# Kernel tuning notes

Hardware: AMD Instinct MI355X
Metric: run time of the kernel (lower is better)

## Reference

```python
import jax, jax.numpy as jnp
import numpy as np

N, F_IN, F_OUT, N_HEAD = 4096, 256, 64, 4
EDGE_P = 0.01  # sparsity of the random adjacency


def setup_inputs() -> dict:
    key = jax.random.key(0)
    k_h, k_adj, k_w, k_as, k_ad = jax.random.split(key, 5)
    h = jax.random.normal(k_h, (N, F_IN), dtype=jnp.float32)
    # random boolean adjacency with self-loops so every softmax row is valid
    adj = jax.random.uniform(k_adj, (N, N)) < EDGE_P
    adj = adj | jnp.eye(N, dtype=bool)
    # xavier_uniform-style params
    lim_w = float(np.sqrt(6.0 / (F_IN + F_OUT)))
    lim_a = float(np.sqrt(6.0 / (F_OUT + 1)))
    w = jax.random.uniform(k_w, (N_HEAD, F_IN, F_OUT), minval=-lim_w, maxval=lim_w, dtype=jnp.float32)
    a_src = jax.random.uniform(k_as, (N_HEAD, F_OUT, 1), minval=-lim_a, maxval=lim_a, dtype=jnp.float32)
    a_dst = jax.random.uniform(k_ad, (N_HEAD, F_OUT, 1), minval=-lim_a, maxval=lim_a, dtype=jnp.float32)
    bias = jnp.zeros((F_OUT,), dtype=jnp.float32)
    return {"h": h, "adj": adj, "w": w, "a_src": a_src, "a_dst": a_dst, "bias": bias}


def reference(h, adj, w, a_src, a_dst, bias):
    # h_prime[k] = h @ w[k]  -> [H, n, f_out]
    h_prime = jnp.einsum('nf,hfo->hno', h, w)
    # attention logits: attn[k,i,j] = src[k,i] + dst[k,j]
    src = jnp.einsum('hno,ho->hn', h_prime, a_src[..., 0])  # [H, n]
    dst = jnp.einsum('hno,ho->hn', h_prime, a_dst[..., 0])  # [H, n]
    scores = src[:, :, None] + dst[:, None, :]              # [H, n, n]
    scores = jnp.where(scores >= 0, scores, 0.2 * scores)   # leaky_relu(0.2)
    neg = jnp.asarray(jnp.finfo(scores.dtype).min, scores.dtype)
    scores = jnp.where(adj[None, :, :], scores, neg)
    attn = jax.nn.softmax(scores, axis=-1)                  # [H, n, n]
    out = jnp.einsum('hij,hjo->iho', attn, h_prime)         # [n, H, f_out]
    return out + bias
```

## Files before the change

### kernel.cpp

```cpp
#include <hip/hip_runtime.h>

#define NN 4096
#define FIN 256
#define FOUT 64
#define NH 4
#define CAP 128
#define MFB 256
#define CPB 1024

typedef __attribute__((ext_vector_type(8))) short bf16x8;
typedef __attribute__((ext_vector_type(4))) float f32x4;

__device__ __forceinline__ unsigned short f2bf(float f) {
    unsigned u = __float_as_uint(f);
    u = (u + 0x7fff + ((u >> 16) & 1)) >> 16;
    return (unsigned short)u;
}
__device__ __forceinline__ float bf2f(unsigned short s) {
    return __uint_as_float((unsigned)s << 16);
}

__global__ __launch_bounds__(256) void gat_prep(
    const float* __restrict__ h, const int* __restrict__ adj,
    const float* __restrict__ w, const float* __restrict__ a_src,
    const float* __restrict__ a_dst,
    unsigned short* __restrict__ hb, float* __restrict__ sd,
    unsigned long long* __restrict__ bits)
{
    const int b = blockIdx.x, t = threadIdx.x;
    const int wv = t >> 6, lane = t & 63;

    __shared__ bf16x8 bfrag[2048];

    if (b < MFB) {
        const int head = b & 3, n0 = (b >> 2) * 64;
        const int lrow = lane & 15, lk8 = lane >> 4;

        const float* hrow = h + (size_t)(n0 + wv * 16 + lrow) * FIN + lk8 * 8;
        bf16x8 a[8];
#pragma unroll
        for (int ks = 0; ks < 8; ++ks) {
            const float4 v0 = *(const float4*)(hrow + ks * 32);
            const float4 v1 = *(const float4*)(hrow + ks * 32 + 4);
            union { bf16x8 v; unsigned short s[8]; } u;
            u.s[0] = f2bf(v0.x); u.s[1] = f2bf(v0.y);
            u.s[2] = f2bf(v0.z); u.s[3] = f2bf(v0.w);
            u.s[4] = f2bf(v1.x); u.s[5] = f2bf(v1.y);
            u.s[6] = f2bf(v1.z); u.s[7] = f2bf(v1.w);
            a[ks] = u.v;
        }

#pragma unroll
        for (int i = 0; i < 8; ++i) {
            const int g = t + i * 256;
            const int lg = g & 63, ks = (g >> 6) & 7, nt = g >> 9;
            const int col = nt * 16 + (lg & 15);
            const int kbase = ks * 32 + (lg >> 4) * 8;
            const float* wp = w + ((size_t)head * FIN + kbase) * FOUT + col;
            union { bf16x8 v; unsigned short s[8]; } u;
#pragma unroll
            for (int j = 0; j < 8; ++j) u.s[j] = f2bf(wp[j * FOUT]);
            bfrag[g] = u.v;
        }
        __syncthreads();

        f32x4 acc[4] = {{0.f,0.f,0.f,0.f},{0.f,0.f,0.f,0.f},
                        {0.f,0.f,0.f,0.f},{0.f,0.f,0.f,0.f}};
#pragma unroll
        for (int ks = 0; ks < 8; ++ks) {
#pragma unroll
            for (int nt = 0; nt < 4; ++nt)
                acc[nt] = __builtin_amdgcn_mfma_f32_16x16x32_bf16(
                              a[ks], bfrag[(nt * 8 + ks) * 64 + lane], acc[nt], 0, 0, 0);
        }

        const int mbase = n0 + wv * 16 + lk8 * 4;
#pragma unroll
        for (int nt = 0; nt < 4; ++nt)
#pragma unroll
            for (int r = 0; r < 4; ++r)
                hb[((size_t)head * NN + mbase + r) * FOUT + nt * 16 + lrow] =
                    f2bf(acc[nt][r]);

        float as_nt[4], ad_nt[4];
#pragma unroll
        for (int nt = 0; nt < 4; ++nt) {
            as_nt[nt] = a_src[head * FOUT + nt * 16 + lrow];
            ad_nt[nt] = a_dst[head * FOUT + nt * 16 + lrow];
        }
        float psr[4] = {0.f,0.f,0.f,0.f}, pdr[4] = {0.f,0.f,0.f,0.f};
#pragma unroll
        for (int nt = 0; nt < 4; ++nt)
#pragma unroll
            for (int r = 0; r < 4; ++r) {
                psr[r] = fmaf(acc[nt][r], as_nt[nt], psr[r]);
                pdr[r] = fmaf(acc[nt][r], ad_nt[nt], pdr[r]);
            }
#pragma unroll
        for (int r = 0; r < 4; ++r)
#pragma unroll
            for (int off = 1; off <= 8; off <<= 1) {
                psr[r] += __shfl_xor(psr[r], off, 64);
                pdr[r] += __shfl_xor(pdr[r], off, 64);
            }
        if (lrow == 0)
#pragma unroll
            for (int r = 0; r < 4; ++r) {
                sd[(size_t)(mbase + r) * 8 + head]     = psr[r];
                sd[(size_t)(mbase + r) * 8 + 4 + head] = pdr[r];
            }
    } else {
        const int row = (b - MFB) * 4 + wv;
        const int4* arow = (const int4*)(adj + (size_t)row * NN);
        int4 buf[16];
#pragma unroll
        for (int it = 0; it < 16; ++it) buf[it] = arow[it * 64 + lane];

        unsigned long long* brow = bits + (size_t)row * 64;
#pragma unroll
        for (int it = 0; it < 16; ++it) {
            const unsigned long long b0 = __ballot(buf[it].x != 0);
            const unsigned long long b1 = __ballot(buf[it].y != 0);
            const unsigned long long b2 = __ballot(buf[it].z != 0);
            const unsigned long long b3 = __ballot(buf[it].w != 0);
            unsigned long long mk = b0;
            mk = ((lane & 3) == 1) ? b1 : mk;
            mk = ((lane & 3) == 2) ? b2 : mk;
            mk = ((lane & 3) == 3) ? b3 : mk;
            if (lane < 4) brow[it * 4 + lane] = mk;
        }
    }
}

__global__ __launch_bounds__(256) void gat_attn(
    const unsigned long long* __restrict__ bits,
    const unsigned short* __restrict__ hb, const float* __restrict__ sd,
    const float* __restrict__ bias, float* __restrict__ out)
{
    const int i = blockIdx.x, t = threadIdx.x, wv = t >> 6, lane = t & 63;

    __shared__ int   idx_l[CAP];
    __shared__ float sc[NH][CAP];
    __shared__ int   cnt;
    __shared__ float inv_sum[NH];

    if (wv == 0) {
        unsigned long long m = bits[(size_t)i * 64 + lane];
        const int c = __popcll(m);
        int pre = c;
#pragma unroll
        for (int off = 1; off < 64; off <<= 1) {
            const int nb = __shfl_up(pre, off, 64);
            if (lane >= off) pre += nb;
        }
        int p = pre - c;
        const int cb = (lane >> 2) * 256 + (lane & 3);
        while (m) {
            const int bpos = __ffsll((unsigned long long)m) - 1;
            if (p < CAP) idx_l[p] = cb + 4 * bpos;
            ++p;
            m &= m - 1;
        }
        if (lane == 63) cnt = pre;
    }
    __syncthreads();

    const int count = min(cnt, CAP);
    const int cpad  = (count + 7) & ~7;

    if (t < count) {
        const int j = idx_l[t];
        const float4 sv = *(const float4*)(sd + (size_t)i * 8);
        const float4 dv = *(const float4*)(sd + (size_t)j * 8 + 4);
        const float s0 = sv.x + dv.x, s1 = sv.y + dv.y;
        const float s2 = sv.z + dv.z, s3 = sv.w + dv.w;
        sc[0][t] = (s0 >= 0.f) ? s0 : 0.2f * s0;
        sc[1][t] = (s1 >= 0.f) ? s1 : 0.2f * s1;
        sc[2][t] = (s2 >= 0.f) ? s2 : 0.2f * s2;
        sc[3][t] = (s3 >= 0.f) ? s3 : 0.2f * s3;
    } else if (t < cpad) {
        idx_l[t] = 0;
#pragma unroll
        for (int hh = 0; hh < NH; ++hh) sc[hh][t] = 0.f;
    }
    __syncthreads();

    {
        float m = -3.4e38f;
        for (int p = lane; p < count; p += 64) m = fmaxf(m, sc[wv][p]);
#pragma unroll
        for (int off = 32; off >= 1; off >>= 1) m = fmaxf(m, __shfl_xor(m, off, 64));
        float e = 0.f;
        for (int p = lane; p < count; p += 64) {
            const float v = __expf(sc[wv][p] - m);
            sc[wv][p] = v;
            e += v;
        }
#pragma unroll
        for (int off = 32; off >= 1; off >>= 1) e += __shfl_xor(e, off, 64);
        if (lane == 0) inv_sum[wv] = 1.f / e;
    }
    __syncthreads();

    float accv = 0.f;
    const unsigned short* hp = hb + (size_t)(wv * NN) * FOUT + lane;
    for (int p0 = 0; p0 < cpad; p0 += 8) {
        int jj[8]; unsigned short vv[8]; float ww[8];
#pragma unroll
        for (int k = 0; k < 8; ++k) jj[k] = idx_l[p0 + k];
#pragma unroll
        for (int k = 0; k < 8; ++k) vv[k] = hp[(size_t)jj[k] * FOUT];
#pragma unroll
        for (int k = 0; k < 8; ++k) ww[k] = sc[wv][p0 + k];
#pragma unroll
        for (int k = 0; k < 8; ++k) accv = fmaf(ww[k], bf2f(vv[k]), accv);
    }
    out[(size_t)i * (NH * FOUT) + wv * FOUT + lane] = accv * inv_sum[wv] + bias[lane];
}

extern "C" void kernel_launch(void* const* d_in, const int* in_sizes, int n_in,
                              void* d_out, int out_size, void* d_ws, size_t ws_size,
                              hipStream_t stream) {
    const float* h     = (const float*)d_in[0];
    const int*   adj   = (const int*)d_in[1];
    const float* w     = (const float*)d_in[2];
    const float* a_src = (const float*)d_in[3];
    const float* a_dst = (const float*)d_in[4];
    const float* bias  = (const float*)d_in[5];
    float* out = (float*)d_out;

    unsigned short* hb = (unsigned short*)d_ws;
    float* sd          = (float*)(hb + (size_t)NH * NN * FOUT);
    unsigned long long* bits = (unsigned long long*)(sd + (size_t)NN * 8);

    gat_prep<<<MFB + CPB, 256, 0, stream>>>(h, adj, w, a_src, a_dst, hb, sd, bits);
    gat_attn<<<NN, 256, 0, stream>>>(bits, hb, sd, bias, out);
}
```

Baseline: 35.86 us.

## Fuse adjacency compaction into attention kernel, drop bitmask intermediate

Moves the adjacency-to-index compaction out of the prep kernel and into the per-row attention kernel. Each block now reads its own adjacency row directly, building the neighbor list with ballots and mbcnt-based prefix offsets across four waves. This removes the bitmask write and read through global memory and shrinks the prep grid to the matmul blocks only. In exchange, the adjacency read, which dominates traffic, now sits on the attention kernel's critical path and no longer overlaps with the matmul blocks. Each attention block also gains an extra barrier.

Result: no change. 35.27 us (-1.6%).

```diff
diff --git a/kernel.cpp b/kernel.cpp
--- a/kernel.cpp
+++ b/kernel.cpp
@@ -5,8 +5,6 @@
 #define FOUT 64
 #define NH 4
 #define CAP 128
-#define MFB 256
-#define CPB 1024
 
 typedef __attribute__((ext_vector_type(8))) short bf16x8;
 typedef __attribute__((ext_vector_type(4))) float f32x4;
@@ -19,154 +17,149 @@
 __device__ __forceinline__ float bf2f(unsigned short s) {
     return __uint_as_float((unsigned)s << 16);
 }
-
-__global__ __launch_bounds__(256) void gat_prep(
-    const float* __restrict__ h, const int* __restrict__ adj,
-    const float* __restrict__ w, const float* __restrict__ a_src,
-    const float* __restrict__ a_dst,
-    unsigned short* __restrict__ hb, float* __restrict__ sd,
-    unsigned long long* __restrict__ bits)
+__device__ __forceinline__ int mbcnt64(unsigned long long m) {
+    return __builtin_amdgcn_mbcnt_hi((unsigned)(m >> 32),
+           __builtin_amdgcn_mbcnt_lo((unsigned)m, 0));
+}
+
+__global__ __launch_bounds__(256) void gat_mfma(
+    const float* __restrict__ h, const float* __restrict__ w,
+    const float* __restrict__ a_src, const float* __restrict__ a_dst,
+    unsigned short* __restrict__ hb, float* __restrict__ sd)
 {
     const int b = blockIdx.x, t = threadIdx.x;
     const int wv = t >> 6, lane = t & 63;
+    const int head = b & 3, n0 = (b >> 2) * 64;
+    const int lrow = lane & 15, lk8 = lane >> 4;
 
     __shared__ bf16x8 bfrag[2048];
 
-    if (b < MFB) {
-        const int head = b & 3, n0 = (b >> 2) * 64;
-        const int lrow = lane & 15, lk8 = lane >> 4;
-
-        const float* hrow = h + (size_t)(n0 + wv * 16 + lrow) * FIN + lk8 * 8;
-        bf16x8 a[8];
-#pragma unroll
-        for (int ks = 0; ks < 8; ++ks) {
-            const float4 v0 = *(const float4*)(hrow + ks * 32);
-            const float4 v1 = *(const float4*)(hrow + ks * 32 + 4);
-            union { bf16x8 v; unsigned short s[8]; } u;
-            u.s[0] = f2bf(v0.x); u.s[1] = f2bf(v0.y);
-            u.s[2] = f2bf(v0.z); u.s[3] = f2bf(v0.w);
-            u.s[4] = f2bf(v1.x); u.s[5] = f2bf(v1.y);
-            u.s[6] = f2bf(v1.z); u.s[7] = f2bf(v1.w);
-            a[ks] = u.v;
-        }
-
-#pragma unroll
-        for (int i = 0; i < 8; ++i) {
-            const int g = t + i * 256;
-            const int lg = g & 63, ks = (g >> 6) & 7, nt = g >> 9;
-            const int col = nt * 16 + (lg & 15);
-            const int kbase = ks * 32 + (lg >> 4) * 8;
-            const float* wp = w + ((size_t)head * FIN + kbase) * FOUT + col;
-            union { bf16x8 v; unsigned short s[8]; } u;
-#pragma unroll
-            for (int j = 0; j < 8; ++j) u.s[j] = f2bf(wp[j * FOUT]);
-            bfrag[g] = u.v;
-        }
-        __syncthreads();
-
-        f32x4 acc[4] = {{0.f,0.f,0.f,0.f},{0.f,0.f,0.f,0.f},
-                        {0.f,0.f,0.f,0.f},{0.f,0.f,0.f,0.f}};
-#pragma unroll
-        for (int ks = 0; ks < 8; ++ks) {
-#pragma unroll
-            for (int nt = 0; nt < 4; ++nt)
-                acc[nt] = __builtin_amdgcn_mfma_f32_16x16x32_bf16(
-                              a[ks], bfrag[(nt * 8 + ks) * 64 + lane], acc[nt], 0, 0, 0);
-        }
-
-        const int mbase = n0 + wv * 16 + lk8 * 4;
+    const float* hrow = h + (size_t)(n0 + wv * 16 + lrow) * FIN + lk8 * 8;
+    bf16x8 a[8];
+#pragma unroll
+    for (int ks = 0; ks < 8; ++ks) {
+        const float4 v0 = *(const float4*)(hrow + ks * 32);
+        const float4 v1 = *(const float4*)(hrow + ks * 32 + 4);
+        union { bf16x8 v; unsigned short s[8]; } u;
+        u.s[0] = f2bf(v0.x); u.s[1] = f2bf(v0.y);
+        u.s[2] = f2bf(v0.z); u.s[3] = f2bf(v0.w);
+        u.s[4] = f2bf(v1.x); u.s[5] = f2bf(v1.y);
+        u.s[6] = f2bf(v1.z); u.s[7] = f2bf(v1.w);
+        a[ks] = u.v;
+    }
+
+#pragma unroll
+    for (int i = 0; i < 8; ++i) {
+        const int g = t + i * 256;
+        const int lg = g & 63, ks = (g >> 6) & 7, nt = g >> 9;
+        const int col = nt * 16 + (lg & 15);
+        const int kbase = ks * 32 + (lg >> 4) * 8;
+        const float* wp = w + ((size_t)head * FIN + kbase) * FOUT + col;
+        union { bf16x8 v; unsigned short s[8]; } u;
+#pragma unroll
+        for (int j = 0; j < 8; ++j) u.s[j] = f2bf(wp[j * FOUT]);
+        bfrag[g] = u.v;
+    }
+    __syncthreads();
+
+    f32x4 acc[4] = {{0.f,0.f,0.f,0.f},{0.f,0.f,0.f,0.f},
+                    {0.f,0.f,0.f,0.f},{0.f,0.f,0.f,0.f}};
+#pragma unroll
+    for (int ks = 0; ks < 8; ++ks) {
 #pragma unroll
         for (int nt = 0; nt < 4; ++nt)
-#pragma unroll
-            for (int r = 0; r < 4; ++r)
-                hb[((size_t)head * NN + mbase + r) * FOUT + nt * 16 + lrow] =
-                    f2bf(acc[nt][r]);
-
-        float as_nt[4], ad_nt[4];
-#pragma unroll
-        for (int nt = 0; nt < 4; ++nt) {
-            as_nt[nt] = a_src[head * FOUT + nt * 16 + lrow];
-            ad_nt[nt] = a_dst[head * FOUT + nt * 16 + lrow];
-        }
-        float psr[4] = {0.f,0.f,0.f,0.f}, pdr[4] = {0.f,0.f,0.f,0.f};
-#pragma unroll
-        for (int nt = 0; nt < 4; ++nt)
-#pragma unroll
-            for (int r = 0; r < 4; ++r) {
-                psr[r] = fmaf(acc[nt][r], as_nt[nt], psr[r]);
-                pdr[r] = fmaf(acc[nt][r], ad_nt[nt], pdr[r]);
-            }
+            acc[nt] = __builtin_amdgcn_mfma_f32_16x16x32_bf16(
+                          a[ks], bfrag[(nt * 8 + ks) * 64 + lane], acc[nt], 0, 0, 0);
+    }
+
+    const int mbase = n0 + wv * 16 + lk8 * 4;
+#pragma unroll
+    for (int nt = 0; nt < 4; ++nt)
 #pragma unroll
         for (int r = 0; r < 4; ++r)
-#pragma unroll
-            for (int off = 1; off <= 8; off <<= 1) {
-                psr[r] += __shfl_xor(psr[r], off, 64);
-                pdr[r] += __shfl_xor(pdr[r], off, 64);
-            }
-        if (lrow == 0)
-#pragma unroll
-            for (int r = 0; r < 4; ++r) {
-                sd[(size_t)(mbase + r) * 8 + head]     = psr[r];
-                sd[(size_t)(mbase + r) * 8 + 4 + head] = pdr[r];
-            }
-    } else {
-        const int row = (b - MFB) * 4 + wv;
-        const int4* arow = (const int4*)(adj + (size_t)row * NN);
-        int4 buf[16];
-#pragma unroll
-        for (int it = 0; it < 16; ++it) buf[it] = arow[it * 64 + lane];
-
-        unsigned long long* brow = bits + (size_t)row * 64;
-#pragma unroll
-        for (int it = 0; it < 16; ++it) {
-            const unsigned long long b0 = __ballot(buf[it].x != 0);
-            const unsigned long long b1 = __ballot(buf[it].y != 0);
-            const unsigned long long b2 = __ballot(buf[it].z != 0);
-            const unsigned long long b3 = __ballot(buf[it].w != 0);
-            unsigned long long mk = b0;
-            mk = ((lane & 3) == 1) ? b1 : mk;
-            mk = ((lane & 3) == 2) ? b2 : mk;
-            mk = ((lane & 3) == 3) ? b3 : mk;
-            if (lane < 4) brow[it * 4 + lane] = mk;
-        }
-    }
+            hb[((size_t)head * NN + mbase + r) * FOUT + nt * 16 + lrow] =
+                f2bf(acc[nt][r]);
+
+    float as_nt[4], ad_nt[4];
+#pragma unroll
+    for (int nt = 0; nt < 4; ++nt) {
+        as_nt[nt] = a_src[head * FOUT + nt * 16 + lrow];
+        ad_nt[nt] = a_dst[head * FOUT + nt * 16 + lrow];
+    }
+    float psr[4] = {0.f,0.f,0.f,0.f}, pdr[4] = {0.f,0.f,0.f,0.f};
+#pragma unroll
+    for (int nt = 0; nt < 4; ++nt)
+#pragma unroll
+        for (int r = 0; r < 4; ++r) {
+            psr[r] = fmaf(acc[nt][r], as_nt[nt], psr[r]);
+            pdr[r] = fmaf(acc[nt][r], ad_nt[nt], pdr[r]);
+        }
+#pragma unroll
+    for (int r = 0; r < 4; ++r)
+#pragma unroll
+        for (int off = 1; off <= 8; off <<= 1) {
+            psr[r] += __shfl_xor(psr[r], off, 64);
+            pdr[r] += __shfl_xor(pdr[r], off, 64);
+        }
+    if (lrow == 0)
+#pragma unroll
+        for (int r = 0; r < 4; ++r) {
+            sd[(size_t)(mbase + r) * 8 + head]     = psr[r];
+            sd[(size_t)(mbase + r) * 8 + 4 + head] = pdr[r];
+        }
 }
 
 __global__ __launch_bounds__(256) void gat_attn(
-    const unsigned long long* __restrict__ bits,
-    const unsigned short* __restrict__ hb, const float* __restrict__ sd,
-    const float* __restrict__ bias, float* __restrict__ out)
+    const int* __restrict__ adj, const unsigned short* __restrict__ hb,
+    const float* __restrict__ sd, const float* __restrict__ bias,
+    float* __restrict__ out)
 {
     const int i = blockIdx.x, t = threadIdx.x, wv = t >> 6, lane = t & 63;
 
     __shared__ int   idx_l[CAP];
     __shared__ float sc[NH][CAP];
-    __shared__ int   cnt;
+    __shared__ int   ccnt[16];
     __shared__ float inv_sum[NH];
 
-    if (wv == 0) {
-        unsigned long long m = bits[(size_t)i * 64 + lane];
-        const int c = __popcll(m);
-        int pre = c;
-#pragma unroll
-        for (int off = 1; off < 64; off <<= 1) {
-            const int nb = __shfl_up(pre, off, 64);
-            if (lane >= off) pre += nb;
-        }
-        int p = pre - c;
-        const int cb = (lane >> 2) * 256 + (lane & 3);
-        while (m) {
-            const int bpos = __ffsll((unsigned long long)m) - 1;
-            if (p < CAP) idx_l[p] = cb + 4 * bpos;
-            ++p;
-            m &= m - 1;
-        }
-        if (lane == 63) cnt = pre;
-    }
-    __syncthreads();
-
-    const int count = min(cnt, CAP);
+    const int4* arow = (const int4*)(adj + (size_t)i * NN);
+    int4 a[4];
+#pragma unroll
+    for (int it = 0; it < 4; ++it) a[it] = arow[wv * 256 + it * 64 + lane];
+
+    int myoff[4];
+#pragma unroll
+    for (int it = 0; it < 4; ++it) {
+        const unsigned long long b0 = __ballot(a[it].x != 0);
+        const unsigned long long b1 = __ballot(a[it].y != 0);
+        const unsigned long long b2 = __ballot(a[it].z != 0);
+        const unsigned long long b3 = __ballot(a[it].w != 0);
+        myoff[it] = mbcnt64(b0) + mbcnt64(b1) + mbcnt64(b2) + mbcnt64(b3);
+        if (lane == 0)
+            ccnt[wv * 4 + it] = __popcll(b0) + __popcll(b1) +
+                                __popcll(b2) + __popcll(b3);
+    }
+    __syncthreads();
+
+    int cb[4];
+    int s = 0;
+#pragma unroll
+    for (int k = 0; k < 16; ++k) {
+        if ((k >> 2) == wv) cb[k & 3] = s;
+        s += ccnt[k];
+    }
+    const int count = min(s, CAP);
     const int cpad  = (count + 7) & ~7;
+
+#pragma unroll
+    for (int it = 0; it < 4; ++it) {
+        int p = cb[it] + myoff[it];
+        const int col0 = (wv * 256 + it * 64 + lane) * 4;
+        if (a[it].x) { if (p < CAP) idx_l[p] = col0;     ++p; }
+        if (a[it].y) { if (p < CAP) idx_l[p] = col0 + 1; ++p; }
+        if (a[it].z) { if (p < CAP) idx_l[p] = col0 + 2; ++p; }
+        if (a[it].w) { if (p < CAP) idx_l[p] = col0 + 3; ++p; }
+    }
+    __syncthreads();
 
     if (t < count) {
         const int j = idx_l[t];
@@ -231,8 +224,7 @@
 
     unsigned short* hb = (unsigned short*)d_ws;
     float* sd          = (float*)(hb + (size_t)NH * NN * FOUT);
-    unsigned long long* bits = (unsigned long long*)(sd + (size_t)NN * 8);
-
-    gat_prep<<<MFB + CPB, 256, 0, stream>>>(h, adj, w, a_src, a_dst, hb, sd, bits);
-    gat_attn<<<NN, 256, 0, stream>>>(bits, hb, sd, bias, out);
-}
+
+    gat_mfma<<<256, 256, 0, stream>>>(h, w, a_src, a_dst, hb, sd);
+    gat_attn<<<NN, 256, 0, stream>>>(adj, hb, sd, bias, out);
+}
```

## Split prep into separate adjacency bitpack and h-prime GEMM kernels

Applied to the files above, without the earlier changes.

The fused prep kernel is split into a dedicated grid-strided adjacency-to-bitmask kernel (2048 blocks, two int4 loads in flight per iteration) and a separate GEMM kernel. The GEMM kernel now uses 32-row tiles with two waves splitting the output columns, which doubles the block count. It also stages W transposed in padded shared memory with coalesced float4 loads, and combines the src/dst partial sums through shared memory. This aims to raise memory-level parallelism for the 64MB adjacency read and to coalesce the W loads, at the cost of one extra kernel launch and serializing the two prep phases.

Result: slower. 40.57 us (+13.1%).

```diff
diff --git a/kernel.cpp b/kernel.cpp
--- a/kernel.cpp
+++ b/kernel.cpp
@@ -5,8 +5,7 @@
 #define FOUT 64
 #define NH 4
 #define CAP 128
-#define MFB 256
-#define CPB 1024
+#define WROW 258
 
 typedef __attribute__((ext_vector_type(8))) short bf16x8;
 typedef __attribute__((ext_vector_type(4))) float f32x4;
@@ -20,114 +19,138 @@
     return __uint_as_float((unsigned)s << 16);
 }
 
-__global__ __launch_bounds__(256) void gat_prep(
-    const float* __restrict__ h, const int* __restrict__ adj,
-    const float* __restrict__ w, const float* __restrict__ a_src,
-    const float* __restrict__ a_dst,
-    unsigned short* __restrict__ hb, float* __restrict__ sd,
-    unsigned long long* __restrict__ bits)
+__global__ __launch_bounds__(256) void gat_scanbits(
+    const int* __restrict__ adj, unsigned long long* __restrict__ bits)
+{
+    const int lane = threadIdx.x & 63;
+    const int tid  = blockIdx.x * 256 + threadIdx.x;
+    const int STR  = 2048 * 256;
+#pragma unroll
+    for (int it = 0; it < 4; ++it) {
+        const int g0 = tid + (2 * it) * STR;
+        const int g1 = g0 + STR;
+        const int4 a0 = ((const int4*)adj)[g0];
+        const int4 a1 = ((const int4*)adj)[g1];
+
+        const unsigned long long x0 = __ballot(a0.x != 0);
+        const unsigned long long y0 = __ballot(a0.y != 0);
+        const unsigned long long z0 = __ballot(a0.z != 0);
+        const unsigned long long w0 = __ballot(a0.w != 0);
+        unsigned long long m0 = x0;
+        m0 = ((lane & 3) == 1) ? y0 : m0;
+        m0 = ((lane & 3) == 2) ? z0 : m0;
+        m0 = ((lane & 3) == 3) ? w0 : m0;
+        if (lane < 4)
+            bits[(size_t)(g0 >> 10) * 64 + ((g0 >> 6) & 15) * 4 + lane] = m0;
+
+        const unsigned long long x1 = __ballot(a1.x != 0);
+        const unsigned long long y1 = __ballot(a1.y != 0);
+        const unsigned long long z1 = __ballot(a1.z != 0);
+        const unsigned long long w1 = __ballot(a1.w != 0);
+        unsigned long long m1 = x1;
+        m1 = ((lane & 3) == 1) ? y1 : m1;
+        m1 = ((lane & 3) == 2) ? z1 : m1;
+        m1 = ((lane & 3) == 3) ? w1 : m1;
+        if (lane < 4)
+            bits[(size_t)(g1 >> 10) * 64 + ((g1 >> 6) & 15) * 4 + lane] = m1;
+    }
+}
+
+__global__ __launch_bounds__(256) void gat_hprime(
+    const float* __restrict__ h, const float* __restrict__ w,
+    const float* __restrict__ a_src, const float* __restrict__ a_dst,
+    unsigned short* __restrict__ hb, float* __restrict__ sd)
 {
     const int b = blockIdx.x, t = threadIdx.x;
+    const int head = b & 3, n0 = (b >> 2) * 32;
     const int wv = t >> 6, lane = t & 63;
-
-    __shared__ bf16x8 bfrag[2048];
-
-    if (b < MFB) {
-        const int head = b & 3, n0 = (b >> 2) * 64;
-        const int lrow = lane & 15, lk8 = lane >> 4;
-
-        const float* hrow = h + (size_t)(n0 + wv * 16 + lrow) * FIN + lk8 * 8;
-        bf16x8 a[8];
-#pragma unroll
-        for (int ks = 0; ks < 8; ++ks) {
-            const float4 v0 = *(const float4*)(hrow + ks * 32);
-            const float4 v1 = *(const float4*)(hrow + ks * 32 + 4);
-            union { bf16x8 v; unsigned short s[8]; } u;
-            u.s[0] = f2bf(v0.x); u.s[1] = f2bf(v0.y);
-            u.s[2] = f2bf(v0.z); u.s[3] = f2bf(v0.w);
-            u.s[4] = f2bf(v1.x); u.s[5] = f2bf(v1.y);
-            u.s[6] = f2bf(v1.z); u.s[7] = f2bf(v1.w);
-            a[ks] = u.v;
-        }
-
-#pragma unroll
-        for (int i = 0; i < 8; ++i) {
-            const int g = t + i * 256;
-            const int lg = g & 63, ks = (g >> 6) & 7, nt = g >> 9;
-            const int col = nt * 16 + (lg & 15);
-            const int kbase = ks * 32 + (lg >> 4) * 8;
-            const float* wp = w + ((size_t)head * FIN + kbase) * FOUT + col;
-            union { bf16x8 v; unsigned short s[8]; } u;
-#pragma unroll
-            for (int j = 0; j < 8; ++j) u.s[j] = f2bf(wp[j * FOUT]);
-            bfrag[g] = u.v;
-        }
-        __syncthreads();
-
-        f32x4 acc[4] = {{0.f,0.f,0.f,0.f},{0.f,0.f,0.f,0.f},
-                        {0.f,0.f,0.f,0.f},{0.f,0.f,0.f,0.f}};
-#pragma unroll
-        for (int ks = 0; ks < 8; ++ks) {
-#pragma unroll
-            for (int nt = 0; nt < 4; ++nt)
-                acc[nt] = __builtin_amdgcn_mfma_f32_16x16x32_bf16(
-                              a[ks], bfrag[(nt * 8 + ks) * 64 + lane], acc[nt], 0, 0, 0);
-        }
-
-        const int mbase = n0 + wv * 16 + lk8 * 4;
-#pragma unroll
-        for (int nt = 0; nt < 4; ++nt)
-#pragma unroll
-            for (int r = 0; r < 4; ++r)
-                hb[((size_t)head * NN + mbase + r) * FOUT + nt * 16 + lrow] =
-                    f2bf(acc[nt][r]);
-
-        float as_nt[4], ad_nt[4];
-#pragma unroll
-        for (int nt = 0; nt < 4; ++nt) {
-            as_nt[nt] = a_src[head * FOUT + nt * 16 + lrow];
-            ad_nt[nt] = a_dst[head * FOUT + nt * 16 + lrow];
-        }
-        float psr[4] = {0.f,0.f,0.f,0.f}, pdr[4] = {0.f,0.f,0.f,0.f};
-#pragma unroll
-        for (int nt = 0; nt < 4; ++nt)
-#pragma unroll
-            for (int r = 0; r < 4; ++r) {
-                psr[r] = fmaf(acc[nt][r], as_nt[nt], psr[r]);
-                pdr[r] = fmaf(acc[nt][r], ad_nt[nt], pdr[r]);
-            }
+    const int lrow = lane & 15, lk8 = lane >> 4;
+
+    __shared__ __align__(16) unsigned short ws[64 * WROW];
+    __shared__ float sdbuf[2][2][16][2];
+
+#pragma unroll
+    for (int i = 0; i < 16; ++i) {
+        const int k  = (t >> 4) + i * 16;
+        const int o4 = (t & 15) * 4;
+        const float4 v = *(const float4*)(w + ((size_t)head * FIN + k) * FOUT + o4);
+        ws[(o4 + 0) * WROW + k] = f2bf(v.x);
+        ws[(o4 + 1) * WROW + k] = f2bf(v.y);
+        ws[(o4 + 2) * WROW + k] = f2bf(v.z);
+        ws[(o4 + 3) * WROW + k] = f2bf(v.w);
+    }
+
+    const float* hrow = h + (size_t)(n0 + (wv >> 1) * 16 + lrow) * FIN + lk8 * 8;
+    bf16x8 a[8];
+#pragma unroll
+    for (int ks = 0; ks < 8; ++ks) {
+        const float4 v0 = *(const float4*)(hrow + ks * 32);
+        const float4 v1 = *(const float4*)(hrow + ks * 32 + 4);
+        union { bf16x8 v; unsigned short s[8]; } u;
+        u.s[0] = f2bf(v0.x); u.s[1] = f2bf(v0.y);
+        u.s[2] = f2bf(v0.z); u.s[3] = f2bf(v0.w);
+        u.s[4] = f2bf(v1.x); u.s[5] = f2bf(v1.y);
+        u.s[6] = f2bf(v1.z); u.s[7] = f2bf(v1.w);
+        a[ks] = u.v;
+    }
+    __syncthreads();
+
+    const int obase = (wv & 1) * 32;
+    f32x4 acc[2] = {{0.f,0.f,0.f,0.f},{0.f,0.f,0.f,0.f}};
+#pragma unroll
+    for (int ks = 0; ks < 8; ++ks) {
+#pragma unroll
+        for (int nt = 0; nt < 2; ++nt) {
+            const bf16x8 bf = *(const bf16x8*)
+                &ws[(obase + nt * 16 + lrow) * WROW + ks * 32 + lk8 * 8];
+            acc[nt] = __builtin_amdgcn_mfma_f32_16x16x32_bf16(a[ks], bf, acc[nt], 0, 0, 0);
+        }
+    }
+
+    const int mbase = n0 + (wv >> 1) * 16 + lk8 * 4;
+#pragma unroll
+    for (int nt = 0; nt < 2; ++nt)
 #pragma unroll
         for (int r = 0; r < 4; ++r)
-#pragma unroll
-            for (int off = 1; off <= 8; off <<= 1) {
-                psr[r] += __shfl_xor(psr[r], off, 64);
-                pdr[r] += __shfl_xor(pdr[r], off, 64);
-            }
-        if (lrow == 0)
-#pragma unroll
-            for (int r = 0; r < 4; ++r) {
-                sd[(size_t)(mbase + r) * 8 + head]     = psr[r];
-                sd[(size_t)(mbase + r) * 8 + 4 + head] = pdr[r];
-            }
-    } else {
-        const int row = (b - MFB) * 4 + wv;
-        const int4* arow = (const int4*)(adj + (size_t)row * NN);
-        int4 buf[16];
-#pragma unroll
-        for (int it = 0; it < 16; ++it) buf[it] = arow[it * 64 + lane];
-
-        unsigned long long* brow = bits + (size_t)row * 64;
-#pragma unroll
-        for (int it = 0; it < 16; ++it) {
-            const unsigned long long b0 = __ballot(buf[it].x != 0);
-            const unsigned long long b1 = __ballot(buf[it].y != 0);
-            const unsigned long long b2 = __ballot(buf[it].z != 0);
-            const unsigned long long b3 = __ballot(buf[it].w != 0);
-            unsigned long long mk = b0;
-            mk = ((lane & 3) == 1) ? b1 : mk;
-            mk = ((lane & 3) == 2) ? b2 : mk;
-            mk = ((lane & 3) == 3) ? b3 : mk;
-            if (lane < 4) brow[it * 4 + lane] = mk;
+            hb[((size_t)head * NN + mbase + r) * FOUT + obase + nt * 16 + lrow] =
+                f2bf(acc[nt][r]);
+
+    float as_nt[2], ad_nt[2];
+#pragma unroll
+    for (int nt = 0; nt < 2; ++nt) {
+        as_nt[nt] = a_src[head * FOUT + obase + nt * 16 + lrow];
+        ad_nt[nt] = a_dst[head * FOUT + obase + nt * 16 + lrow];
+    }
+    float psr[4] = {0.f,0.f,0.f,0.f}, pdr[4] = {0.f,0.f,0.f,0.f};
+#pragma unroll
+    for (int nt = 0; nt < 2; ++nt)
+#pragma unroll
+        for (int r = 0; r < 4; ++r) {
+            psr[r] = fmaf(acc[nt][r], as_nt[nt], psr[r]);
+            pdr[r] = fmaf(acc[nt][r], ad_nt[nt], pdr[r]);
+        }
+#pragma unroll
+    for (int r = 0; r < 4; ++r)
+#pragma unroll
+        for (int off = 1; off <= 8; off <<= 1) {
+            psr[r] += __shfl_xor(psr[r], off, 64);
+            pdr[r] += __shfl_xor(pdr[r], off, 64);
+        }
+    if (lrow == 0)
+#pragma unroll
+        for (int r = 0; r < 4; ++r) {
+            sdbuf[wv >> 1][wv & 1][lk8 * 4 + r][0] = psr[r];
+            sdbuf[wv >> 1][wv & 1][lk8 * 4 + r][1] = pdr[r];
+        }
+    __syncthreads();
+    if ((wv & 1) == 0 && lrow == 0) {
+        const int p = wv >> 1;
+#pragma unroll
+        for (int r = 0; r < 4; ++r) {
+            const int n = lk8 * 4 + r;
+            const int node = n0 + p * 16 + n;
+            sd[(size_t)node * 8 + head]     = sdbuf[p][0][n][0] + sdbuf[p][1][n][0];
+            sd[(size_t)node * 8 + 4 + head] = sdbuf[p][0][n][1] + sdbuf[p][1][n][1];
         }
     }
 }
@@ -233,6 +256,7 @@
     float* sd          = (float*)(hb + (size_t)NH * NN * FOUT);
     unsigned long long* bits = (unsigned long long*)(sd + (size_t)NN * 8);
 
-    gat_prep<<<MFB + CPB, 256, 0, stream>>>(h, adj, w, a_src, a_dst, hb, sd, bits);
+    gat_scanbits<<<2048, 256, 0, stream>>>(adj, bits);
+    gat_hprime<<<512, 256, 0, stream>>>(h, w, a_src, a_dst, hb, sd);
     gat_attn<<<NN, 256, 0, stream>>>(bits, hb, sd, bias, out);
 }
```
